# Kernel tuning notes

Measured on AMD Instinct MI355X. Metric: run time of the kernel, lower is better.

## Reference

```python
import jax, jax.numpy as jnp
import numpy as np

D_K = 64
NEG = -1e9

def setup_inputs() -> dict:
    key = jax.random.key(0)
    kq, kk, kv, km = jax.random.split(key, 4)
    B, H, S, Dk, Dv = 4, 16, 1024, D_K, 64
    Q = jax.random.normal(kq, (B, H, S, Dk), dtype=jnp.float32)
    K = jax.random.normal(kk, (B, H, S, Dk), dtype=jnp.float32)
    V = jax.random.normal(kv, (B, H, S, Dv), dtype=jnp.float32)
    attn_mask = jax.random.randint(km, (B, H, S, S), 0, 2).astype(bool)
    return {"Q": Q, "K": K, "V": V, "attn_mask": attn_mask}

def reference(Q, K, V, attn_mask):
    # scores: [B, H, Sq, Sk]
    scores = jnp.einsum('bhqd,bhkd->bhqk', Q, K) / np.sqrt(D_K).astype(np.float32)
    scores = jnp.where(attn_mask, jnp.float32(NEG), scores)
    attn = jax.nn.softmax(scores, axis=-1)
    context = jnp.einsum('bhqk,bhkv->bhqv', attn, V)
    return (context, attn)
```

## Files before the change

### kernel.cpp

```cpp
#include <hip/hip_runtime.h>
#include <hip/hip_bf16.h>

#define S_LEN 1024
#define DK 64
#define NW 8

typedef __attribute__((ext_vector_type(8))) short bf16x8;
typedef __attribute__((ext_vector_type(16))) float f32x16;
typedef __attribute__((ext_vector_type(4))) float f32x4;

__device__ __forceinline__ unsigned short f2bf(float f) {
    __hip_bfloat16 h = __float2bfloat16(f);
    unsigned short u; __builtin_memcpy(&u, &h, 2);
    return u;
}
__device__ __forceinline__ bf16x8 load_cvt8(const float* p, float scale) {
    float4 a = *(const float4*)p;
    float4 b = *(const float4*)(p + 4);
    bf16x8 r;
    r[0] = (short)f2bf(a.x * scale); r[1] = (short)f2bf(a.y * scale);
    r[2] = (short)f2bf(a.z * scale); r[3] = (short)f2bf(a.w * scale);
    r[4] = (short)f2bf(b.x * scale); r[5] = (short)f2bf(b.y * scale);
    r[6] = (short)f2bf(b.z * scale); r[7] = (short)f2bf(b.w * scale);
    return r;
}

__global__ __launch_bounds__(256)
void prep_kernel(const float* __restrict__ K, const float* __restrict__ V,
                 unsigned short* __restrict__ wsK, unsigned short* __restrict__ wsV)
{
    const int b = blockIdx.x;
    const int head = b >> 5, kblk = b & 31;
    const int tid = threadIdx.x;
    const int l = tid & 63, c = tid >> 6;

    {
        const float* src = K + ((size_t)(head * S_LEN) + kblk * 32 + (l & 31)) * DK
                             + c * 16 + (l >> 5) * 8;
        bf16x8 r = load_cvt8(src, 1.f);
        *(bf16x8*)(wsK + (((size_t)(head * 32 + kblk) * 4 + c) * 64 + l) * 8) = r;
    }
    {
        const int ktl = c & 1, dt = c >> 1;
        const int kt = kblk * 2 + ktl;
        const float* src = V + ((size_t)(head * S_LEN) + kt * 16 + (l >> 5) * 8) * DK
                             + (l & 31) + 32 * dt;
        bf16x8 r;
#pragma unroll
        for (int j = 0; j < 8; ++j) r[j] = (short)f2bf(src[j * DK]);
        *(bf16x8*)(wsV + (((size_t)(head * 64 + kt) * 2 + dt) * 64 + l) * 8) = r;
    }
}

__global__ __launch_bounds__(512, 2)
void sdpa_kernel(const float* __restrict__ Q, const int* __restrict__ M,
                 const unsigned short* __restrict__ wsK,
                 const unsigned short* __restrict__ wsV,
                 float* __restrict__ OC, float* __restrict__ OA)
{
    __shared__ unsigned long long mlds[32 * 17];
    __shared__ unsigned short    plds[NW * 32 * 64];
    __shared__ float             cbuf[32 * DK];
    __shared__ float             wsum[32];

    const int bid  = blockIdx.x;
    const int lin  = (bid & 7) * 256 + (bid >> 3);
    const int head = lin >> 5;
    const int q0   = (lin & 31) * 32;

    const int tid  = threadIdx.x;
    const int wv   = tid >> 6;
    const int lane = tid & 63;
    const int lo   = tid & 31;
    const int hi   = (tid >> 5) & 1;

    *(float4*)(cbuf + tid * 4) = float4{0.f, 0.f, 0.f, 0.f};
    if (tid < 32) wsum[tid] = 0.f;

    const float* qptr = Q + (size_t)(head * S_LEN + q0 + lo) * DK + hi * 8;
    bf16x8 qf[4];
#pragma unroll
    for (int s = 0; s < 4; ++s) qf[s] = load_cvt8(qptr + s * 16, 0.125f);

    {
        const int* mb = M + (size_t)(head * S_LEN + q0 + wv * 4) * S_LEN;
#pragma unroll
        for (int r4 = 0; r4 < 4; ++r4) {
            int mv[16];
#pragma unroll
            for (int s = 0; s < 16; ++s)
                mv[s] = __builtin_nontemporal_load(mb + r4 * S_LEN + s * 64 + lane);
            unsigned long long bal[16];
#pragma unroll
            for (int s = 0; s < 16; ++s) bal[s] = __ballot(mv[s] != 0);
            if (lane == 0) {
#pragma unroll
                for (int s = 0; s < 16; ++s) mlds[(wv * 4 + r4) * 17 + s] = bal[s];
            }
        }
    }

    f32x16 acc[4];
#pragma unroll
    for (int t = 0; t < 4; ++t) {
        const unsigned short* kp = wsK + ((size_t)(head * 32 + wv * 4 + t) * 4 * 64 + lane) * 8;
        f32x16 a;
#pragma unroll
        for (int i = 0; i < 16; ++i) a[i] = 0.f;
#pragma unroll
        for (int s = 0; s < 4; ++s) {
            bf16x8 kf = *(const bf16x8*)(kp + (size_t)s * 64 * 8);
            a = __builtin_amdgcn_mfma_f32_32x32x16_bf16(qf[s], kf, a, 0, 0, 0);
        }
        acc[t] = a;
    }

    __syncthreads();

    const unsigned* m32 = (const unsigned*)mlds;
    float rs[16];
#pragma unroll
    for (int r = 0; r < 16; ++r) rs[r] = 0.f;
#pragma unroll
    for (int t = 0; t < 4; ++t) {
#pragma unroll
        for (int r = 0; r < 16; ++r) {
            const int row = (r & 3) + 8 * (r >> 2) + 4 * hi;
            const unsigned mw = m32[row * 34 + wv * 4 + t];
            const float e = ((mw >> lo) & 1u) ? 0.f : __expf(acc[t][r]);
            acc[t][r] = e;
            rs[r] += e;
        }
    }

#pragma unroll
    for (int r = 0; r < 16; ++r) {
        float v = rs[r];
        v += __shfl_xor(v, 1, 64);
        v += __shfl_xor(v, 2, 64);
        v += __shfl_xor(v, 4, 64);
        v += __shfl_xor(v, 8, 64);
        v += __shfl_xor(v, 16, 64);
        if (lo == 0) atomicAdd(&wsum[(r & 3) + 8 * (r >> 2) + 4 * hi], v);
    }
    __syncthreads();

    float* arow = OA + (size_t)(head * S_LEN + q0) * S_LEN;
#pragma unroll
    for (int r = 0; r < 16; ++r) {
        const int row = (r & 3) + 8 * (r >> 2) + 4 * hi;
        const float iv = __builtin_amdgcn_rcpf(wsum[row]);
        float* ar = arow + (size_t)row * S_LEN + wv * 128 + lo;
#pragma unroll
        for (int t = 0; t < 4; ++t) {
            const float pn = acc[t][r] * iv;
            acc[t][r] = pn;
            __builtin_nontemporal_store(pn, ar + t * 32);
        }
    }

    unsigned short* Pw = plds + wv * (32 * 64);
    f32x16 pvT0, pvT1;
#pragma unroll
    for (int i = 0; i < 16; ++i) { pvT0[i] = 0.f; pvT1[i] = 0.f; }

#pragma unroll
    for (int h = 0; h < 2; ++h) {
#pragma unroll
        for (int t2 = 0; t2 < 2; ++t2) {
            const int t = h * 2 + t2;
#pragma unroll
            for (int r = 0; r < 16; ++r) {
                const int row = (r & 3) + 8 * (r >> 2) + 4 * hi;
                const int off = (row * 128 + (t2 * 32 + lo) * 2) ^ ((row & 7) << 4);
                *(unsigned short*)((char*)Pw + off) = f2bf(acc[t][r]);
            }
        }
#pragma unroll
        for (int st2 = 0; st2 < 4; ++st2) {
            const int off = (lo * 128 + st2 * 32 + hi * 16) ^ ((lo & 7) << 4);
            bf16x8 pf = *(const bf16x8*)((const char*)Pw + off);
            const int kt = wv * 8 + h * 4 + st2;
            const unsigned short* vp = wsV + ((size_t)(head * 64 + kt) * 2 * 64 + lane) * 8;
            bf16x8 vf0 = *(const bf16x8*)(vp);
            bf16x8 vf1 = *(const bf16x8*)(vp + 64 * 8);
            pvT0 = __builtin_amdgcn_mfma_f32_32x32x16_bf16(vf0, pf, pvT0, 0, 0, 0);
            pvT1 = __builtin_amdgcn_mfma_f32_32x32x16_bf16(vf1, pf, pvT1, 0, 0, 0);
        }
    }

#pragma unroll
    for (int r = 0; r < 16; ++r) {
        const int d0 = (r & 3) + 8 * (r >> 2) + 4 * hi;
        atomicAdd(&cbuf[lo * DK + ((d0)      ^ ((lo & 15) << 2))], pvT0[r]);
        atomicAdd(&cbuf[lo * DK + ((d0 + 32) ^ ((lo & 15) << 2))], pvT1[r]);
    }
    __syncthreads();

    {
        const int q  = tid >> 4;
        const int d4 = (tid * 4) & 63;
        const int pc = d4 ^ ((q & 15) << 2);
        f32x4 s4 = *(const f32x4*)(cbuf + q * DK + pc);
        __builtin_nontemporal_store(s4, (f32x4*)(OC + (size_t)(head * S_LEN + q0 + q) * DK + d4));
    }
}

extern "C" void kernel_launch(void* const* d_in, const int* in_sizes, int n_in,
                              void* d_out, int out_size, void* d_ws, size_t ws_size,
                              hipStream_t stream) {
    const float* Q = (const float*)d_in[0];
    const float* K = (const float*)d_in[1];
    const float* V = (const float*)d_in[2];
    const int*   M = (const int*)d_in[3];
    float* OC = (float*)d_out;
    float* OA = OC + 4 * 16 * 1024 * 64;
    unsigned short* wsK = (unsigned short*)d_ws;
    unsigned short* wsV = wsK + (size_t)64 * 1024 * 64;
    prep_kernel<<<dim3(2048), dim3(256), 0, stream>>>(K, V, wsK, wsV);
    sdpa_kernel<<<dim3(2048), dim3(512), 0, stream>>>(Q, M, wsK, wsV, OC, OA);
}
```

Before: 313.5 us.

## Restructure PV stage into single pass with un-transposed MFMA and raise occupancy hint

Normalized probabilities are written to LDS as bf16 directly inside the attention-store loop, so the separate acc rescale and two-phase staging disappear. The PV product then runs in one 8-step loop with P as the A operand, which yields an un-transposed output that is atomically added to cbuf without swizzling. The launch bound is raised to 4 blocks per CU to cut register use, with the P scratch buffer doubled in size. The larger LDS footprint may keep the extra occupancy from being reached, and the tighter register limit may cause spills.

```diff
diff --git a/kernel.cpp b/kernel.cpp
--- a/kernel.cpp
+++ b/kernel.cpp
@@ -52,14 +52,14 @@
     }
 }
 
-__global__ __launch_bounds__(512, 2)
+__global__ __launch_bounds__(512, 4)
 void sdpa_kernel(const float* __restrict__ Q, const int* __restrict__ M,
                  const unsigned short* __restrict__ wsK,
                  const unsigned short* __restrict__ wsV,
                  float* __restrict__ OC, float* __restrict__ OA)
 {
     __shared__ unsigned long long mlds[32 * 17];
-    __shared__ unsigned short    plds[NW * 32 * 64];
+    __shared__ unsigned short    plds[NW * 32 * 128];
     __shared__ float             cbuf[32 * DK];
     __shared__ float             wsum[32];
 
@@ -146,6 +146,7 @@
     __syncthreads();
 
     float* arow = OA + (size_t)(head * S_LEN + q0) * S_LEN;
+    unsigned short* Pw = plds + wv * (32 * 128);
 #pragma unroll
     for (int r = 0; r < 16; ++r) {
         const int row = (r & 3) + 8 * (r >> 2) + 4 * hi;
@@ -154,55 +155,40 @@
 #pragma unroll
         for (int t = 0; t < 4; ++t) {
             const float pn = acc[t][r] * iv;
-            acc[t][r] = pn;
             __builtin_nontemporal_store(pn, ar + t * 32);
-        }
-    }
-
-    unsigned short* Pw = plds + wv * (32 * 64);
-    f32x16 pvT0, pvT1;
-#pragma unroll
-    for (int i = 0; i < 16; ++i) { pvT0[i] = 0.f; pvT1[i] = 0.f; }
-
-#pragma unroll
-    for (int h = 0; h < 2; ++h) {
-#pragma unroll
-        for (int t2 = 0; t2 < 2; ++t2) {
-            const int t = h * 2 + t2;
-#pragma unroll
-            for (int r = 0; r < 16; ++r) {
-                const int row = (r & 3) + 8 * (r >> 2) + 4 * hi;
-                const int off = (row * 128 + (t2 * 32 + lo) * 2) ^ ((row & 7) << 4);
-                *(unsigned short*)((char*)Pw + off) = f2bf(acc[t][r]);
-            }
-        }
-#pragma unroll
-        for (int st2 = 0; st2 < 4; ++st2) {
-            const int off = (lo * 128 + st2 * 32 + hi * 16) ^ ((lo & 7) << 4);
-            bf16x8 pf = *(const bf16x8*)((const char*)Pw + off);
-            const int kt = wv * 8 + h * 4 + st2;
-            const unsigned short* vp = wsV + ((size_t)(head * 64 + kt) * 2 * 64 + lane) * 8;
-            bf16x8 vf0 = *(const bf16x8*)(vp);
-            bf16x8 vf1 = *(const bf16x8*)(vp + 64 * 8);
-            pvT0 = __builtin_amdgcn_mfma_f32_32x32x16_bf16(vf0, pf, pvT0, 0, 0, 0);
-            pvT1 = __builtin_amdgcn_mfma_f32_32x32x16_bf16(vf1, pf, pvT1, 0, 0, 0);
-        }
+            const int off = (row * 256 + (t * 32 + lo) * 2) ^ ((row & 15) << 4);
+            *(unsigned short*)((char*)Pw + off) = f2bf(pn);
+        }
+    }
+
+    f32x16 pv0, pv1;
+#pragma unroll
+    for (int i = 0; i < 16; ++i) { pv0[i] = 0.f; pv1[i] = 0.f; }
+#pragma unroll
+    for (int st = 0; st < 8; ++st) {
+        const int off = (lo * 256 + st * 32 + hi * 16) ^ ((lo & 15) << 4);
+        bf16x8 af = *(const bf16x8*)((const char*)Pw + off);
+        const int kt = wv * 8 + st;
+        const unsigned short* vp = wsV + ((size_t)(head * 64 + kt) * 2 * 64 + lane) * 8;
+        bf16x8 vf0 = *(const bf16x8*)(vp);
+        bf16x8 vf1 = *(const bf16x8*)(vp + 64 * 8);
+        pv0 = __builtin_amdgcn_mfma_f32_32x32x16_bf16(af, vf0, pv0, 0, 0, 0);
+        pv1 = __builtin_amdgcn_mfma_f32_32x32x16_bf16(af, vf1, pv1, 0, 0, 0);
     }
 
 #pragma unroll
     for (int r = 0; r < 16; ++r) {
-        const int d0 = (r & 3) + 8 * (r >> 2) + 4 * hi;
-        atomicAdd(&cbuf[lo * DK + ((d0)      ^ ((lo & 15) << 2))], pvT0[r]);
-        atomicAdd(&cbuf[lo * DK + ((d0 + 32) ^ ((lo & 15) << 2))], pvT1[r]);
+        const int q = (r & 3) + 8 * (r >> 2) + 4 * hi;
+        atomicAdd(&cbuf[q * DK + lo], pv0[r]);
+        atomicAdd(&cbuf[q * DK + 32 + lo], pv1[r]);
     }
     __syncthreads();
 
     {
-        const int q  = tid >> 4;
-        const int d4 = (tid * 4) & 63;
-        const int pc = d4 ^ ((q & 15) << 2);
-        f32x4 s4 = *(const f32x4*)(cbuf + q * DK + pc);
-        __builtin_nontemporal_store(s4, (f32x4*)(OC + (size_t)(head * S_LEN + q0 + q) * DK + d4));
+        f32x4 s4 = *(const f32x4*)(cbuf + tid * 4);
+        const int row = tid >> 4;
+        const int col = (tid * 4) & 63;
+        __builtin_nontemporal_store(s4, (f32x4*)(OC + (size_t)(head * S_LEN + q0 + row) * DK + col));
     }
 }
 
```

After: 312.5 us. Within noise of the previous version (-0.3%).
